# Kernel tuning notes

Hardware: AMD Instinct MI355X
Metric: run time of the kernel (lower is better)

The kernel has to match this reference:

```python
import jax, jax.numpy as jnp
import numpy as np

NUM_CLASSES = 10
BATCH = 2048
DIM = 128
TEMPERATURE = 0.07
BASE_TEMPERATURE = 0.07


def setup_inputs() -> dict:
    key = jax.random.key(0)
    k1, k2 = jax.random.split(key)
    preds = jax.random.normal(k1, (NUM_CLASSES, BATCH, DIM), dtype=jnp.float32)
    target = jax.random.randint(k2, (BATCH,), 0, NUM_CLASSES, dtype=jnp.int64)
    log_vars = jnp.zeros((NUM_CLASSES,), dtype=jnp.float32)
    return {"preds": preds, "target": target, "log_vars": log_vars}


def _per_class_loss(features, labels_bin):
    # features: [B, D], labels_bin: [B] in {0,1} (target == class i)
    B = features.shape[0]
    mask = (labels_bin[:, None] == labels_bin[None, :]).astype(features.dtype)  # [B,B]
    logits_mask = 1.0 - jnp.eye(B, dtype=features.dtype)                        # zero diagonal
    sim = jnp.matmul(features, features.T) / TEMPERATURE                        # [B,B]
    norms = jnp.linalg.norm(features, axis=1, keepdims=True)                    # [B,1]
    logits = sim / (norms * norms.T)                                            # cosine / temp
    mask = mask * logits_mask
    exp_logits = jnp.exp(logits) * logits_mask
    log_prob = logits - jnp.log(exp_logits.sum(axis=1, keepdims=True))
    mean_log_prob_pos = (mask * log_prob).sum(axis=1) / mask.sum(axis=1)
    loss = -(TEMPERATURE / BASE_TEMPERATURE) * mean_log_prob_pos
    return loss.mean()


def reference(preds, target, log_vars):
    # labels_bin[i] = (target == i), one row per class
    labels_bin = (target[None, :] == jnp.arange(NUM_CLASSES, dtype=target.dtype)[:, None])
    losses = jax.vmap(_per_class_loss)(preds, labels_bin)  # [num_classes]
    final_loss = jnp.sum(jnp.exp(-log_vars) * losses + log_vars)
    return final_loss
```

## Files before the change

kernel.cpp:

```cpp
#include <hip/hip_runtime.h>
#include <hip/hip_bf16.h>
#include <math.h>

#define NUM_CLASSES 10
#define BATCH 2048
#define DIM 128
#define INV_T 14.285714285714286f
#define NTILE 16
#define NPAIR 136

typedef __attribute__((ext_vector_type(8))) short bf16x8;
typedef __attribute__((ext_vector_type(4))) float f32x4;

__device__ __forceinline__ void load_lds16(const void* g, void* lds) {
    __builtin_amdgcn_global_load_lds(
        (const __attribute__((address_space(1))) unsigned int*)g,
        (__attribute__((address_space(3))) unsigned int*)lds,
        16, 0, 0);
}

__global__ __launch_bounds__(256) void normalize_kernel(
    const float* __restrict__ preds, __hip_bfloat16* __restrict__ g,
    const float* __restrict__ log_vars, float* __restrict__ out)
{
    int b = blockIdx.x;
    int t = threadIdx.x;
    if (b == 0 && t == 0) {
        float lv = 0.0f;
        for (int i = 0; i < NUM_CLASSES; ++i) lv += log_vars[i];
        out[0] = lv;
    }

    int row  = b * 4 + (t >> 6);
    int lane = t & 63;
    const float2* src = (const float2*)(preds + (size_t)row * DIM);
    float2 v = src[lane];
    float ss = v.x * v.x + v.y * v.y;
#pragma unroll
    for (int m = 32; m; m >>= 1) ss += __shfl_xor(ss, m, 64);
    float rn = 1.0f / sqrtf(ss);
    __hip_bfloat162 o;
    o.x = __float2bfloat16(v.x * rn);
    o.y = __float2bfloat16(v.y * rn);
    *(__hip_bfloat162*)(g + (size_t)row * DIM + lane * 2) = o;
}

__global__ __launch_bounds__(256) void gram_kernel(
    const __hip_bfloat16* __restrict__ g, const int* __restrict__ target,
    float2* __restrict__ part)
{
    int p = blockIdx.x;
    int by = 0, rem = NTILE;
    while (p >= rem) { p -= rem; --rem; ++by; }
    const int bx   = by + p;
    const int cls  = blockIdx.y;
    const int row0 = by * 128;
    const int col0 = bx * 128;
    const bool isDiag = (by == bx);
    const ushort* gc = (const ushort*)g + (size_t)cls * BATCH * DIM;

    __shared__ __align__(16) ushort smem[2 * 128 * 128];
    ushort* As = smem;
    ushort* Bs = smem + 128 * 128;

    const int t    = threadIdx.x;
    const int wid  = t >> 6;
    const int lane = t & 63;
    const int tx   = lane & 15;
    const int quad = lane >> 4;
    const int wm   = (wid >> 1) * 64;
    const int wn   = (wid & 1) * 64;

    const int lr = lane >> 4;
    const int lp = lane & 15;
#pragma unroll
    for (int s = 0; s < 8; ++s) {
        int rb = s * 16 + wid * 4;
        int r  = rb + lr;
        int c  = lp ^ (r & 15);
        load_lds16(gc + (size_t)(row0 + r) * DIM + c * 8, &As[rb * 128]);
        if (!isDiag)
            load_lds16(gc + (size_t)(col0 + r) * DIM + c * 8, &Bs[rb * 128]);
    }
    __syncthreads();

    const ushort* BsR = isDiag ? As : Bs;
    f32x4 acc[4][4] = {};
#pragma unroll
    for (int ks = 0; ks < 4; ++ks) {
        bf16x8 af[4], bg[4];
#pragma unroll
        for (int i = 0; i < 4; ++i) {
            int pa = ((ks * 4 + quad) ^ tx) * 8;
            af[i] = *(const bf16x8*)&As [(wm + i * 16 + tx) * 128 + pa];
            bg[i] = *(const bf16x8*)&BsR[(wn + i * 16 + tx) * 128 + pa];
        }
#pragma unroll
        for (int i = 0; i < 4; ++i)
#pragma unroll
            for (int j = 0; j < 4; ++j)
                acc[i][j] = __builtin_amdgcn_mfma_f32_16x16x32_bf16(
                    af[i], bg[j], acc[i][j], 0, 0, 0);
    }
    __syncthreads();

    unsigned laMask = 0;
#pragma unroll
    for (int i = 0; i < 4; ++i)
#pragma unroll
        for (int r = 0; r < 4; ++r)
            if (target[row0 + wm + i * 16 + quad * 4 + r] == cls)
                laMask |= 1u << (i * 4 + r);
    int lb[4];
#pragma unroll
    for (int j = 0; j < 4; ++j) lb[j] = (target[col0 + wn + j * 16 + tx] == cls);

    float2* rbuf = (float2*)smem;
    float2* cbuf = (float2*)(smem + 17408);
    float2 pcol[4] = {};

#pragma unroll
    for (int i = 0; i < 4; ++i) {
        float2 prow[4] = {};
#pragma unroll
        for (int j = 0; j < 4; ++j) {
            int cg = col0 + wn + j * 16 + tx;
            int lbj = lb[j];
#pragma unroll
            for (int r = 0; r < 4; ++r) {
                int rg = row0 + wm + i * 16 + quad * 4 + r;
                float logit = acc[i][j][r] * INV_T;
                float e = __expf(logit);
                bool dg = isDiag && (cg == rg);
                e = dg ? 0.0f : e;
                bool same = (((laMask >> (i * 4 + r)) & 1) == (unsigned)lbj) && !dg;
                float sl = same ? logit : 0.0f;
                prow[r].x += e; prow[r].y += sl;
                pcol[j].x += e; pcol[j].y += sl;
            }
        }
#pragma unroll
        for (int r = 0; r < 4; ++r)
            rbuf[wid * 1088 + (i * 16 + quad * 4 + r) * 17 + tx] = prow[r];
    }
#pragma unroll
    for (int j = 0; j < 4; ++j)
        cbuf[wid * 320 + (j * 16 + tx) * 5 + quad] = pcol[j];
    __syncthreads();

    if (t < 128) {
        int rl = t & 63, grp = t >> 6;
        float den = 0.0f, sp = 0.0f;
#pragma unroll
        for (int w = 0; w < 2; ++w) {
            int base = (2 * grp + w) * 1088 + rl * 17;
#pragma unroll
            for (int x = 0; x < 16; ++x) {
                float2 v = rbuf[base + x];
                den += v.x; sp += v.y;
            }
        }
        part[((size_t)(cls * NTILE + bx)) * BATCH + row0 + t] = make_float2(den, sp);
    } else if (!isDiag) {
        int u = t - 128;
        int cl = u & 63, grp = u >> 6;
        float den = 0.0f, sp = 0.0f;
#pragma unroll
        for (int w = 0; w < 2; ++w) {
            int base = (grp + 2 * w) * 320 + cl * 5;
#pragma unroll
            for (int q = 0; q < 4; ++q) {
                float2 v = cbuf[base + q];
                den += v.x; sp += v.y;
            }
        }
        part[((size_t)(cls * NTILE + by)) * BATCH + col0 + u] = make_float2(den, sp);
    }
}

__global__ __launch_bounds__(256) void final_kernel(
    const float2* __restrict__ part, const int* __restrict__ target,
    const float* __restrict__ log_vars, float* __restrict__ out)
{
    __shared__ int cw[4];
    __shared__ float wred[4];
    const int t   = threadIdx.x;
    const int idx = blockIdx.x * 256 + t;
    const int cls = idx >> 11;
    const int a   = idx & (BATCH - 1);

    int c = 0;
#pragma unroll
    for (int k = 0; k < 8; ++k) c += (target[t * 8 + k] == cls);
#pragma unroll
    for (int m = 1; m < 64; m <<= 1) c += __shfl_xor(c, m, 64);
    if ((t & 63) == 0) cw[t >> 6] = c;
    __syncthreads();
    const int c1 = cw[0] + cw[1] + cw[2] + cw[3];

    float den = 0.0f, sp = 0.0f;
#pragma unroll
    for (int s = 0; s < NTILE; ++s) {
        float2 v = part[((size_t)(cls * NTILE + s)) * BATCH + a];
        den += v.x; sp += v.y;
    }

    const int la  = (target[a] == cls);
    const int cnt = la ? (c1 - 1) : (BATCH - c1 - 1);
    float mlpp = sp / (float)cnt - logf(den);
    float prt = __expf(-log_vars[cls]) * mlpp;
#pragma unroll
    for (int m = 32; m; m >>= 1) prt += __shfl_xor(prt, m, 64);
    if ((t & 63) == 0) wred[t >> 6] = prt;
    __syncthreads();
    if (t == 0)
        atomicAdd(out, -(wred[0] + wred[1] + wred[2] + wred[3]) / (float)BATCH);
}

extern "C" void kernel_launch(void* const* d_in, const int* in_sizes, int n_in,
                              void* d_out, int out_size, void* d_ws, size_t ws_size,
                              hipStream_t stream)
{
    const float* preds    = (const float*)d_in[0];
    const int*   target   = (const int*)  d_in[1];
    const float* log_vars = (const float*)d_in[2];
    float* out = (float*)d_out;

    __hip_bfloat16* gbf = (__hip_bfloat16*)d_ws;
    float2* part = (float2*)((char*)d_ws +
                             (size_t)NUM_CLASSES * BATCH * DIM * 2);

    normalize_kernel<<<NUM_CLASSES * BATCH / 4, 256, 0, stream>>>(
        preds, gbf, log_vars, out);
    gram_kernel<<<dim3(NPAIR, NUM_CLASSES), 256, 0, stream>>>(gbf, target, part);
    final_kernel<<<NUM_CLASSES * BATCH / 256, 256, 0, stream>>>(
        part, target, log_vars, out);
}
```

Before: 86.16 us.

## Compute positive-logit sums via class-sum vectors instead of inside the gram epilogue

The sum of same-label logits for each row is a linear function, so it is rewritten as a dot product of the row with per-class summed feature vectors, minus the row's own squared norm. The normalize kernel now also writes per-stripe partial sums of all rows and of positive rows, plus each row's bf16 squared norm. The gram epilogue then only accumulates the exp denominators, which drops the label loads, the masking and half of the partial-buffer traffic. The final kernel reduces the stripe partials and does a 128-length dot per row, adding extra work to that kernel and a small numeric difference from summing bf16 values in a different order.

Result: slower. 91.69 us (+6.4%).

```diff
diff --git a/kernel.cpp b/kernel.cpp
--- a/kernel.cpp
+++ b/kernel.cpp
@@ -8,6 +8,7 @@
 #define INV_T 14.285714285714286f
 #define NTILE 16
 #define NPAIR 136
+#define VSTRIPE 64
 
 typedef __attribute__((ext_vector_type(8))) short bf16x8;
 typedef __attribute__((ext_vector_type(4))) float f32x4;
@@ -20,34 +21,65 @@
 }
 
 __global__ __launch_bounds__(256) void normalize_kernel(
-    const float* __restrict__ preds, __hip_bfloat16* __restrict__ g,
-    const float* __restrict__ log_vars, float* __restrict__ out)
-{
-    int b = blockIdx.x;
-    int t = threadIdx.x;
-    if (b == 0 && t == 0) {
+    const float* __restrict__ preds, const int* __restrict__ target,
+    __hip_bfloat16* __restrict__ g, float* __restrict__ norm2,
+    float* __restrict__ vpart, const float* __restrict__ log_vars,
+    float* __restrict__ out)
+{
+    const int cls = blockIdx.y;
+    const int st  = blockIdx.x;
+    const int t   = threadIdx.x;
+    if (st == 0 && cls == 0 && t == 0) {
         float lv = 0.0f;
         for (int i = 0; i < NUM_CLASSES; ++i) lv += log_vars[i];
         out[0] = lv;
     }
 
-    int row  = b * 4 + (t >> 6);
-    int lane = t & 63;
-    const float2* src = (const float2*)(preds + (size_t)row * DIM);
-    float2 v = src[lane];
-    float ss = v.x * v.x + v.y * v.y;
-#pragma unroll
-    for (int m = 32; m; m >>= 1) ss += __shfl_xor(ss, m, 64);
-    float rn = 1.0f / sqrtf(ss);
-    __hip_bfloat162 o;
-    o.x = __float2bfloat16(v.x * rn);
-    o.y = __float2bfloat16(v.y * rn);
-    *(__hip_bfloat162*)(g + (size_t)row * DIM + lane * 2) = o;
+    const int wid  = t >> 6;
+    const int lane = t & 63;
+    const int rbase = st * 32 + wid * 8;
+
+    float aAllx = 0.0f, aAlly = 0.0f, a1x = 0.0f, a1y = 0.0f;
+#pragma unroll
+    for (int rr = 0; rr < 8; ++rr) {
+        const int r = rbase + rr;
+        const float2 v =
+            ((const float2*)(preds + ((size_t)cls * BATCH + r) * DIM))[lane];
+        float ss = v.x * v.x + v.y * v.y;
+#pragma unroll
+        for (int m = 32; m; m >>= 1) ss += __shfl_xor(ss, m, 64);
+        float rn = 1.0f / sqrtf(ss);
+        __hip_bfloat162 o;
+        o.x = __float2bfloat16(v.x * rn);
+        o.y = __float2bfloat16(v.y * rn);
+        *(__hip_bfloat162*)(g + ((size_t)cls * BATCH + r) * DIM + lane * 2) = o;
+
+        float gx = __bfloat162float(o.x);
+        float gy = __bfloat162float(o.y);
+        float nn = gx * gx + gy * gy;
+#pragma unroll
+        for (int m = 32; m; m >>= 1) nn += __shfl_xor(nn, m, 64);
+        if (lane == 0) norm2[cls * BATCH + r] = nn;
+
+        aAllx += gx; aAlly += gy;
+        if (target[r] == cls) { a1x += gx; a1y += gy; }
+    }
+
+    __shared__ float vv[4][2][DIM];
+    vv[wid][0][lane * 2]     = aAllx;
+    vv[wid][0][lane * 2 + 1] = aAlly;
+    vv[wid][1][lane * 2]     = a1x;
+    vv[wid][1][lane * 2 + 1] = a1y;
+    __syncthreads();
+
+    const int sel = t >> 7;
+    const int d   = t & 127;
+    float s = vv[0][sel][d] + vv[1][sel][d] + vv[2][sel][d] + vv[3][sel][d];
+    vpart[(((size_t)cls * VSTRIPE + st) * 2 + sel) * DIM + d] = s;
 }
 
 __global__ __launch_bounds__(256) void gram_kernel(
-    const __hip_bfloat16* __restrict__ g, const int* __restrict__ target,
-    float2* __restrict__ part)
+    const __hip_bfloat16* __restrict__ g, float* __restrict__ part)
 {
     int p = blockIdx.x;
     int by = 0, rem = NTILE;
@@ -104,39 +136,24 @@
     }
     __syncthreads();
 
-    unsigned laMask = 0;
-#pragma unroll
-    for (int i = 0; i < 4; ++i)
-#pragma unroll
-        for (int r = 0; r < 4; ++r)
-            if (target[row0 + wm + i * 16 + quad * 4 + r] == cls)
-                laMask |= 1u << (i * 4 + r);
-    int lb[4];
-#pragma unroll
-    for (int j = 0; j < 4; ++j) lb[j] = (target[col0 + wn + j * 16 + tx] == cls);
-
-    float2* rbuf = (float2*)smem;
-    float2* cbuf = (float2*)(smem + 17408);
-    float2 pcol[4] = {};
+    float* rbuf = (float*)smem;
+    float* cbuf = (float*)smem + 4352;
+    float pcol[4] = {};
 
 #pragma unroll
     for (int i = 0; i < 4; ++i) {
-        float2 prow[4] = {};
+        float prow[4] = {};
 #pragma unroll
         for (int j = 0; j < 4; ++j) {
             int cg = col0 + wn + j * 16 + tx;
-            int lbj = lb[j];
 #pragma unroll
             for (int r = 0; r < 4; ++r) {
                 int rg = row0 + wm + i * 16 + quad * 4 + r;
-                float logit = acc[i][j][r] * INV_T;
-                float e = __expf(logit);
+                float e = __expf(acc[i][j][r] * INV_T);
                 bool dg = isDiag && (cg == rg);
                 e = dg ? 0.0f : e;
-                bool same = (((laMask >> (i * 4 + r)) & 1) == (unsigned)lbj) && !dg;
-                float sl = same ? logit : 0.0f;
-                prow[r].x += e; prow[r].y += sl;
-                pcol[j].x += e; pcol[j].y += sl;
+                prow[r] += e;
+                pcol[j] += e;
             }
         }
 #pragma unroll
@@ -150,40 +167,37 @@
 
     if (t < 128) {
         int rl = t & 63, grp = t >> 6;
-        float den = 0.0f, sp = 0.0f;
+        float den = 0.0f;
 #pragma unroll
         for (int w = 0; w < 2; ++w) {
             int base = (2 * grp + w) * 1088 + rl * 17;
 #pragma unroll
-            for (int x = 0; x < 16; ++x) {
-                float2 v = rbuf[base + x];
-                den += v.x; sp += v.y;
-            }
-        }
-        part[((size_t)(cls * NTILE + bx)) * BATCH + row0 + t] = make_float2(den, sp);
+            for (int x = 0; x < 16; ++x) den += rbuf[base + x];
+        }
+        part[((size_t)(cls * NTILE + bx)) * BATCH + row0 + t] = den;
     } else if (!isDiag) {
         int u = t - 128;
         int cl = u & 63, grp = u >> 6;
-        float den = 0.0f, sp = 0.0f;
+        float den = 0.0f;
 #pragma unroll
         for (int w = 0; w < 2; ++w) {
             int base = (grp + 2 * w) * 320 + cl * 5;
 #pragma unroll
-            for (int q = 0; q < 4; ++q) {
-                float2 v = cbuf[base + q];
-                den += v.x; sp += v.y;
-            }
-        }
-        part[((size_t)(cls * NTILE + by)) * BATCH + col0 + u] = make_float2(den, sp);
+            for (int q = 0; q < 4; ++q) den += cbuf[base + q];
+        }
+        part[((size_t)(cls * NTILE + by)) * BATCH + col0 + u] = den;
     }
 }
 
 __global__ __launch_bounds__(256) void final_kernel(
-    const float2* __restrict__ part, const int* __restrict__ target,
-    const float* __restrict__ log_vars, float* __restrict__ out)
+    const float* __restrict__ part, const float* __restrict__ vpart,
+    const float* __restrict__ norm2, const __hip_bfloat16* __restrict__ gbf,
+    const int* __restrict__ target, const float* __restrict__ log_vars,
+    float* __restrict__ out)
 {
     __shared__ int cw[4];
     __shared__ float wred[4];
+    __shared__ float vsum[256];
     const int t   = threadIdx.x;
     const int idx = blockIdx.x * 256 + t;
     const int cls = idx >> 11;
@@ -195,17 +209,39 @@
 #pragma unroll
     for (int m = 1; m < 64; m <<= 1) c += __shfl_xor(c, m, 64);
     if ((t & 63) == 0) cw[t >> 6] = c;
+
+    {
+        const int sel = t >> 7, d = t & 127;
+        float s = 0.0f;
+        for (int st = 0; st < VSTRIPE; ++st)
+            s += vpart[(((size_t)cls * VSTRIPE + st) * 2 + sel) * DIM + d];
+        vsum[sel * 128 + d] = s;
+    }
     __syncthreads();
     const int c1 = cw[0] + cw[1] + cw[2] + cw[3];
 
-    float den = 0.0f, sp = 0.0f;
-#pragma unroll
-    for (int s = 0; s < NTILE; ++s) {
-        float2 v = part[((size_t)(cls * NTILE + s)) * BATCH + a];
-        den += v.x; sp += v.y;
-    }
-
-    const int la  = (target[a] == cls);
+    const int la = (target[a] == cls);
+
+    const ushort* gr = (const ushort*)gbf + ((size_t)cls * BATCH + a) * DIM;
+    float dot = 0.0f;
+#pragma unroll
+    for (int k = 0; k < 16; ++k) {
+        bf16x8 ch = *(const bf16x8*)(gr + k * 8);
+#pragma unroll
+        for (int e = 0; e < 8; ++e) {
+            int d = k * 8 + e;
+            float gv = __uint_as_float(((unsigned)(unsigned short)ch[e]) << 16);
+            float vd = la ? vsum[128 + d] : (vsum[d] - vsum[128 + d]);
+            dot = fmaf(gv, vd, dot);
+        }
+    }
+    const float sp = INV_T * (dot - norm2[cls * BATCH + a]);
+
+    float den = 0.0f;
+#pragma unroll
+    for (int s = 0; s < NTILE; ++s)
+        den += part[((size_t)(cls * NTILE + s)) * BATCH + a];
+
     const int cnt = la ? (c1 - 1) : (BATCH - c1 - 1);
     float mlpp = sp / (float)cnt - logf(den);
     float prt = __expf(-log_vars[cls]) * mlpp;
@@ -226,13 +262,18 @@
     const float* log_vars = (const float*)d_in[2];
     float* out = (float*)d_out;
 
-    __hip_bfloat16* gbf = (__hip_bfloat16*)d_ws;
-    float2* part = (float2*)((char*)d_ws +
-                             (size_t)NUM_CLASSES * BATCH * DIM * 2);
-
-    normalize_kernel<<<NUM_CLASSES * BATCH / 4, 256, 0, stream>>>(
-        preds, gbf, log_vars, out);
-    gram_kernel<<<dim3(NPAIR, NUM_CLASSES), 256, 0, stream>>>(gbf, target, part);
+    char* ws = (char*)d_ws;
+    __hip_bfloat16* gbf = (__hip_bfloat16*)ws;
+    ws += (size_t)NUM_CLASSES * BATCH * DIM * 2;
+    float* part  = (float*)ws;
+    ws += (size_t)NUM_CLASSES * NTILE * BATCH * 4;
+    float* vpart = (float*)ws;
+    ws += (size_t)NUM_CLASSES * VSTRIPE * 2 * DIM * 4;
+    float* norm2 = (float*)ws;
+
+    normalize_kernel<<<dim3(VSTRIPE, NUM_CLASSES), 256, 0, stream>>>(
+        preds, target, gbf, norm2, vpart, log_vars, out);
+    gram_kernel<<<dim3(NPAIR, NUM_CLASSES), 256, 0, stream>>>(gbf, part);
     final_kernel<<<NUM_CLASSES * BATCH / 256, 256, 0, stream>>>(
-        part, target, log_vars, out);
-}
+        part, vpart, norm2, gbf, target, log_vars, out);
+}
```
